# Kernel optimization log

Hardware: AMD Instinct MI355X
Metric: run time of the kernel (lower is better)

The kernel has to match this reference:

```python
import jax, jax.numpy as jnp
import numpy as np

B, S, N = 8, 1024, 1024
IMG_DIM, TXT_DIM = 1024, 768
HEAD_DIM, N_HEADS, N_PROJ = 64, 16, 3
INNER = HEAD_DIM * N_HEADS


def setup_inputs() -> dict:
    key = jax.random.key(0)
    ks = jax.random.split(key, 9)

    def xavier(k, shape):
        fan_out, fan_in = shape[-2], shape[-1]
        limit = float(np.sqrt(6.0 / (fan_in + fan_out)))
        return jax.random.uniform(k, shape, jnp.float32, -limit, limit)

    return {
        "img_tokens": jax.random.normal(ks[0], (B, S, IMG_DIM), jnp.float32),
        "txt_tokens": jax.random.normal(ks[1], (B, N, TXT_DIM), jnp.float32),
        "Wq": xavier(ks[2], (INNER, IMG_DIM)),
        "Wk": xavier(ks[3], (INNER, TXT_DIM)),
        "Wv": xavier(ks[4], (INNER, TXT_DIM)),
        "Wq_banks": xavier(ks[5], (N_PROJ, INNER, IMG_DIM)),
        "Wk_banks": xavier(ks[6], (N_PROJ, INNER, TXT_DIM)),
        "Wrq": xavier(ks[7], (N_PROJ, IMG_DIM)),
        "Wrk": xavier(ks[8], (N_PROJ, TXT_DIM)),
    }


def _ste_argmax_route(scores):
    # forward: hard one-hot; backward: softmax gradient (straight-through)
    soft = jax.nn.softmax(scores, axis=-1)
    one_hot = jax.nn.one_hot(jnp.argmax(scores, axis=-1), scores.shape[-1], dtype=scores.dtype)
    return one_hot + soft - jax.lax.stop_gradient(soft)


def _to_heads(x):
    b, l, _ = x.shape
    return x.reshape(b, l, N_HEADS, HEAD_DIM).transpose(0, 2, 1, 3)  # [B,H,L,d]


def reference(img_tokens, txt_tokens, Wq, Wk, Wv, Wq_banks, Wk_banks, Wrq, Wrk):
    Q = jnp.einsum('bsd,id->bsi', img_tokens, Wq)
    K = jnp.einsum('bnd,id->bni', txt_tokens, Wk)
    V = jnp.einsum('bnd,id->bni', txt_tokens, Wv)

    # Query-side routed redundancy projection
    q_scores = jnp.einsum('bsd,pd->bsp', img_tokens, Wrq)  # [B,S,P]
    q_route = _ste_argmax_route(q_scores)
    q_primes = jnp.einsum('bsd,pid->bsip', img_tokens, Wq_banks)  # [B,S,inner,P]
    Q_prime = jnp.einsum('bsip,bsp->bsi', q_primes, q_route)

    # Key-side routed redundancy projection
    k_scores = jnp.einsum('bnd,pd->bnp', txt_tokens, Wrk)
    k_route = _ste_argmax_route(k_scores)
    k_primes = jnp.einsum('bnd,pid->bnip', txt_tokens, Wk_banks)
    K_prime = jnp.einsum('bnip,bnp->bni', k_primes, k_route)

    return (_to_heads(Q), _to_heads(K), _to_heads(V), _to_heads(Q_prime), _to_heads(K_prime))
```

## Files before the change

### kernel.cpp

```cpp
#include <hip/hip_runtime.h>

typedef unsigned short u16;
typedef unsigned int   u32;
typedef __bf16 bf16x8 __attribute__((ext_vector_type(8)));
typedef float  f32x4  __attribute__((ext_vector_type(4)));

#define DEVI __device__ __forceinline__


DEVI u16 f2bf(float f) {
    u32 u = __float_as_uint(f);
    return (u16)((u + 0x7fffu + ((u >> 16) & 1u)) >> 16);
}
DEVI u32 pk2(float lo, float hi) { return (u32)f2bf(lo) | ((u32)f2bf(hi) << 16); }

DEVI void gload16(const u16* g, u16* s) {
    typedef __attribute__((address_space(1))) const unsigned int GU;
    typedef __attribute__((address_space(3))) unsigned int LU;
    __builtin_amdgcn_global_load_lds((GU*)g, (LU*)s, 16, 0, 0);
}

__global__ __launch_bounds__(512)
void route_fused(const float* __restrict__ img, const float* __restrict__ Wrq,
                 int* __restrict__ cntq, int* __restrict__ qlist, u16* __restrict__ imgB,
                 const float* __restrict__ txt, const float* __restrict__ Wrk,
                 int* __restrict__ cntk, int* __restrict__ klist, u16* __restrict__ txtB)
{
    const float* X; const float* Wr; int D; int* cnt; int* list; u16* Xb; int tokbase;
    if (blockIdx.x < 256) { X = img; Wr = Wrq; D = 1024; cnt = cntq; list = qlist; Xb = imgB; tokbase = blockIdx.x * 32; }
    else                  { X = txt; Wr = Wrk; D = 768;  cnt = cntk; list = klist; Xb = txtB; tokbase = (blockIdx.x - 256) * 32; }

    __shared__ int lcnt[3];
    __shared__ int base[3];
    __shared__ u16 tbank[32];
    __shared__ u16 trank[32];

    const int tid  = threadIdx.x;
    const int lane = tid & 63;
    const int wv   = tid >> 6;
    if (tid < 3) lcnt[tid] = 0;
    __syncthreads();

    const float* w0 = Wr;
    const float* w1 = Wr + D;
    const float* w2 = Wr + 2 * D;

    for (int t = 0; t < 4; ++t) {
        const int ltok = wv * 4 + t;
        const int tok  = tokbase + ltok;
        const float* x = X + (size_t)tok * D;
        u16* xb        = Xb + (size_t)tok * D;
        float a0 = 0.f, a1 = 0.f, a2 = 0.f;
        for (int d = lane * 4; d < D; d += 256) {
            float4 xv = *(const float4*)(x + d);
            uint2 pb = { pk2(xv.x, xv.y), pk2(xv.z, xv.w) };
            *(uint2*)(xb + d) = pb;
            float4 v0 = *(const float4*)(w0 + d);
            float4 v1 = *(const float4*)(w1 + d);
            float4 v2 = *(const float4*)(w2 + d);
            a0 += xv.x * v0.x + xv.y * v0.y + xv.z * v0.z + xv.w * v0.w;
            a1 += xv.x * v1.x + xv.y * v1.y + xv.z * v1.z + xv.w * v1.w;
            a2 += xv.x * v2.x + xv.y * v2.y + xv.z * v2.z + xv.w * v2.w;
        }
#pragma unroll
        for (int m = 32; m; m >>= 1) {
            a0 += __shfl_xor(a0, m);
            a1 += __shfl_xor(a1, m);
            a2 += __shfl_xor(a2, m);
        }
        if (lane == 0) {
            int s = 0; float best = a0;
            if (a1 > best) { best = a1; s = 1; }
            if (a2 > best) { best = a2; s = 2; }
            int r = atomicAdd(&lcnt[s], 1);
            tbank[ltok] = (u16)s;
            trank[ltok] = (u16)r;
        }
    }
    __syncthreads();

    if (tid < 3) base[tid] = atomicAdd(&cnt[tid * 32], lcnt[tid]);
    __syncthreads();

    if (tid < 32) {
        int s = tbank[tid];
        list[s * 8192 + base[s] + trank[tid]] = tokbase + tid;
    }
}

__global__ __launch_bounds__(256)
void cvt_weights(const float* __restrict__ Wq, const float* __restrict__ Wk,
                 const float* __restrict__ Wv, const float* __restrict__ Wqb,
                 const float* __restrict__ Wkb,
                 u16* __restrict__ WqB, u16* __restrict__ WkB, u16* __restrict__ WvB,
                 u16* __restrict__ WqbB, u16* __restrict__ WkbB)
{
    int g = blockIdx.x * 256 + threadIdx.x;
    const float* src; u16* dst; int e;
    if (g < 131072)      { src = Wq;  dst = WqB;  e = g; }
    else if (g < 229376) { src = Wk;  dst = WkB;  e = g - 131072; }
    else if (g < 327680) { src = Wv;  dst = WvB;  e = g - 229376; }
    else if (g < 720896) { src = Wqb; dst = WqbB; e = g - 327680; }
    else                 { src = Wkb; dst = WkbB; e = g - 720896; }
    float4 lo = *(const float4*)(src + (size_t)e * 8);
    float4 hi = *(const float4*)(src + (size_t)e * 8 + 4);
    uint4 p = { pk2(lo.x, lo.y), pk2(lo.z, lo.w), pk2(hi.x, hi.y), pk2(hi.z, hi.w) };
    *(uint4*)(dst + (size_t)e * 8) = p;
}

template <int KD>
DEVI void gemm_core(const u16* gA1, const u16* gA2, const u16* gB1, const u16* gB2,
                    u16* As, u16* Bs, int tid, int wv, int lane, f32x4 (&acc)[4][4])
{
    u16* dA1 = As + 8 * tid;
    u16* dA2 = As + 8 * tid + 2048;
    u16* dB1 = Bs + 8 * tid;
    u16* dB2 = Bs + 8 * tid + 2048;
    const int row15 = lane & 15;
    const int quad  = lane >> 4;
    const int wm = (wv & 1) * 64;
    const int wn = (wv >> 1) * 64;

    for (int k0 = 0; k0 < KD; k0 += 32) {
        gload16(gA1 + k0, dA1);
        gload16(gA2 + k0, dA2);
        gload16(gB1 + k0, dB1);
        gload16(gB2 + k0, dB2);
        __syncthreads();

        bf16x8 a[4], b[4];
#pragma unroll
        for (int i = 0; i < 4; ++i)
            a[i] = *(const bf16x8*)(As + (wm + i * 16 + row15) * 32 + quad * 8);
#pragma unroll
        for (int j = 0; j < 4; ++j)
            b[j] = *(const bf16x8*)(Bs + (wn + j * 16 + row15) * 32 + quad * 8);
#pragma unroll
        for (int i = 0; i < 4; ++i)
#pragma unroll
            for (int j = 0; j < 4; ++j)
                acc[i][j] = __builtin_amdgcn_mfma_f32_16x16x32_bf16(a[i], b[j], acc[i][j], 0, 0, 0);
        __syncthreads();
    }
}

template <int KD>
__global__ __launch_bounds__(256)
void gemm_heads(const u16* __restrict__ A, const u16* __restrict__ W, float* __restrict__ out)
{
    __shared__ __align__(16) u16 As[128 * 32];
    __shared__ __align__(16) u16 Bs[128 * 32];
    const int tid  = threadIdx.x;
    const int lane = tid & 63;
    const int wv   = tid >> 6;
    const int rowbase = blockIdx.x * 128;
    const int nbase   = blockIdx.y * 128;
    const int r1   = tid >> 2;
    const int koff = (tid & 3) * 8;

    const u16* gA1 = A + (size_t)(rowbase + r1) * KD + koff;
    const u16* gA2 = A + (size_t)(rowbase + 64 + r1) * KD + koff;
    const u16* gB1 = W + (size_t)(nbase + r1) * KD + koff;
    const u16* gB2 = W + (size_t)(nbase + 64 + r1) * KD + koff;

    f32x4 acc[4][4];
#pragma unroll
    for (int i = 0; i < 4; ++i)
#pragma unroll
        for (int j = 0; j < 4; ++j)
            acc[i][j] = (f32x4){0.f, 0.f, 0.f, 0.f};

    gemm_core<KD>(gA1, gA2, gB1, gB2, As, Bs, tid, wv, lane, acc);

    const int row15 = lane & 15, quad = lane >> 4;
    const int wm = (wv & 1) * 64, wn = (wv >> 1) * 64;
#pragma unroll
    for (int i = 0; i < 4; ++i) {
#pragma unroll
        for (int r = 0; r < 4; ++r) {
            int m = rowbase + wm + i * 16 + quad * 4 + r;
            int bb = m >> 10, l = m & 1023;
#pragma unroll
            for (int j = 0; j < 4; ++j) {
                int n = nbase + wn + j * 16 + row15;
                size_t off = (((size_t)(bb * 16 + (n >> 6)) * 1024) + l) * 64 + (n & 63);
                out[off] = acc[i][j][r];
            }
        }
    }
}

template <int KD>
__global__ __launch_bounds__(256)
void gemm_prime(const u16* __restrict__ A, const u16* __restrict__ Wb,
                const int* __restrict__ cnt, const int* __restrict__ list,
                float* __restrict__ out)
{
    const int c0 = cnt[0], c1 = cnt[32], c2 = cnt[64];
    const int t0 = (c0 + 127) >> 7, t1 = (c1 + 127) >> 7, t2 = (c2 + 127) >> 7;
    const int rt = blockIdx.x;
    int bank, lt, cb;
    if (rt < t0)                { bank = 0; lt = rt;            cb = c0; }
    else if (rt < t0 + t1)      { bank = 1; lt = rt - t0;       cb = c1; }
    else if (rt < t0 + t1 + t2) { bank = 2; lt = rt - t0 - t1;  cb = c2; }
    else return;

    const int* bl = list + bank * 8192;
    const u16* W = Wb + (size_t)bank * 1024 * KD;

    __shared__ __align__(16) u16 As[128 * 32];
    __shared__ __align__(16) u16 Bs[128 * 32];
    const int tid  = threadIdx.x;
    const int lane = tid & 63;
    const int wv   = tid >> 6;
    const int nbase = blockIdx.y * 128;
    const int r1   = tid >> 2;
    const int koff = (tid & 3) * 8;

    int i1 = lt * 128 + r1;       if (i1 >= cb) i1 = cb - 1;
    int i2 = lt * 128 + 64 + r1;  if (i2 >= cb) i2 = cb - 1;
    const u16* gA1 = A + (size_t)bl[i1] * KD + koff;
    const u16* gA2 = A + (size_t)bl[i2] * KD + koff;
    const u16* gB1 = W + (size_t)(nbase + r1) * KD + koff;
    const u16* gB2 = W + (size_t)(nbase + 64 + r1) * KD + koff;

    f32x4 acc[4][4];
#pragma unroll
    for (int i = 0; i < 4; ++i)
#pragma unroll
        for (int j = 0; j < 4; ++j)
            acc[i][j] = (f32x4){0.f, 0.f, 0.f, 0.f};

    gemm_core<KD>(gA1, gA2, gB1, gB2, As, Bs, tid, wv, lane, acc);

    const int row15 = lane & 15, quad = lane >> 4;
    const int wm = (wv & 1) * 64, wn = (wv >> 1) * 64;
#pragma unroll
    for (int i = 0; i < 4; ++i) {
#pragma unroll
        for (int r = 0; r < 4; ++r) {
            int idx = lt * 128 + wm + i * 16 + quad * 4 + r;
            if (idx < cb) {
                int m = bl[idx];
                int bb = m >> 10, l = m & 1023;
#pragma unroll
                for (int j = 0; j < 4; ++j) {
                    int n = nbase + wn + j * 16 + row15;
                    size_t off = (((size_t)(bb * 16 + (n >> 6)) * 1024) + l) * 64 + (n & 63);
                    out[off] = acc[i][j][r];
                }
            }
        }
    }
}

extern "C" void kernel_launch(void* const* d_in, const int* in_sizes, int n_in,
                              void* d_out, int out_size, void* d_ws, size_t ws_size,
                              hipStream_t stream)
{
    const float* img = (const float*)d_in[0];
    const float* txt = (const float*)d_in[1];
    const float* Wq  = (const float*)d_in[2];
    const float* Wk  = (const float*)d_in[3];
    const float* Wv  = (const float*)d_in[4];
    const float* Wqb = (const float*)d_in[5];
    const float* Wkb = (const float*)d_in[6];
    const float* Wrq = (const float*)d_in[7];
    const float* Wrk = (const float*)d_in[8];
    float* out = (float*)d_out;

    int* cntq  = (int*)d_ws;
    int* cntk  = (int*)d_ws + 128;
    int* qlist = (int*)d_ws + 256;
    int* klist = qlist + 3 * 8192;
    u16* imgB  = (u16*)((char*)d_ws + (1 << 18));
    u16* txtB  = imgB + (size_t)8192 * 1024;
    u16* WqB   = txtB + (size_t)8192 * 768;
    u16* WkB   = WqB  + (size_t)1024 * 1024;
    u16* WvB   = WkB  + (size_t)1024 * 768;
    u16* WqbB  = WvB  + (size_t)1024 * 768;
    u16* WkbB  = WqbB + (size_t)3 * 1024 * 1024;

    const size_t OSZ = (size_t)8 * 16 * 1024 * 64;

    hipMemsetAsync(d_ws, 0, 1024, stream);

    route_fused<<<512, 512, 0, stream>>>(img, Wrq, cntq, qlist, imgB,
                                         txt, Wrk, cntk, klist, txtB);
    cvt_weights<<<3968, 256, 0, stream>>>(Wq, Wk, Wv, Wqb, Wkb,
                                          WqB, WkB, WvB, WqbB, WkbB);

    gemm_heads<1024><<<dim3(64, 8), 256, 0, stream>>>(imgB, WqB, out);
    gemm_heads<768> <<<dim3(64, 8), 256, 0, stream>>>(txtB, WkB, out + OSZ);
    gemm_heads<768> <<<dim3(64, 8), 256, 0, stream>>>(txtB, WvB, out + 2 * OSZ);

    gemm_prime<1024><<<dim3(66, 8), 256, 0, stream>>>(imgB, WqbB, cntq, qlist, out + 3 * OSZ);
    gemm_prime<768> <<<dim3(66, 8), 256, 0, stream>>>(txtB, WkbB, cntk, klist, out + 4 * OSZ);
}
```

Before: 414.0 us.

## Merge GEMMs into one launch, deepen K tile to 64 with swizzled LDS

Weight conversion now runs inside the routing kernel as extra blocks, and the five GEMMs (three dense head projections, two routed bank projections) run as a single persistent-grid launch that dispatches on block index. The GEMM core now loads 64-wide K slices, halving barrier count per tile, and XOR-swizzles the LDS layout to avoid bank conflicts on fragment reads. This cuts launch overhead and tail gaps between kernels at the cost of doubled shared memory per block, which may lower occupancy.

```diff
diff --git a/kernel.cpp b/kernel.cpp
--- a/kernel.cpp
+++ b/kernel.cpp
@@ -21,11 +21,33 @@
 }
 
 __global__ __launch_bounds__(512)
-void route_fused(const float* __restrict__ img, const float* __restrict__ Wrq,
-                 int* __restrict__ cntq, int* __restrict__ qlist, u16* __restrict__ imgB,
-                 const float* __restrict__ txt, const float* __restrict__ Wrk,
-                 int* __restrict__ cntk, int* __restrict__ klist, u16* __restrict__ txtB)
-{
+void route_cvt(const float* __restrict__ img, const float* __restrict__ Wrq,
+               int* __restrict__ cntq, int* __restrict__ qlist, u16* __restrict__ imgB,
+               const float* __restrict__ txt, const float* __restrict__ Wrk,
+               int* __restrict__ cntk, int* __restrict__ klist, u16* __restrict__ txtB,
+               const float* __restrict__ Wq, const float* __restrict__ Wk,
+               const float* __restrict__ Wv, const float* __restrict__ Wqb,
+               const float* __restrict__ Wkb,
+               u16* __restrict__ WqB, u16* __restrict__ WkB, u16* __restrict__ WvB,
+               u16* __restrict__ WqbB, u16* __restrict__ WkbB)
+{
+    const int tid = threadIdx.x;
+
+    if (blockIdx.x >= 512) {
+        int g = (blockIdx.x - 512) * 512 + tid;
+        const float* src; u16* dst; int e;
+        if (g < 131072)      { src = Wq;  dst = WqB;  e = g; }
+        else if (g < 229376) { src = Wk;  dst = WkB;  e = g - 131072; }
+        else if (g < 327680) { src = Wv;  dst = WvB;  e = g - 229376; }
+        else if (g < 720896) { src = Wqb; dst = WqbB; e = g - 327680; }
+        else                 { src = Wkb; dst = WkbB; e = g - 720896; }
+        float4 lo = *(const float4*)(src + (size_t)e * 8);
+        float4 hi = *(const float4*)(src + (size_t)e * 8 + 4);
+        uint4 p = { pk2(lo.x, lo.y), pk2(lo.z, lo.w), pk2(hi.x, hi.y), pk2(hi.z, hi.w) };
+        *(uint4*)(dst + (size_t)e * 8) = p;
+        return;
+    }
+
     const float* X; const float* Wr; int D; int* cnt; int* list; u16* Xb; int tokbase;
     if (blockIdx.x < 256) { X = img; Wr = Wrq; D = 1024; cnt = cntq; list = qlist; Xb = imgB; tokbase = blockIdx.x * 32; }
     else                  { X = txt; Wr = Wrk; D = 768;  cnt = cntk; list = klist; Xb = txtB; tokbase = (blockIdx.x - 256) * 32; }
@@ -35,7 +57,6 @@
     __shared__ u16 tbank[32];
     __shared__ u16 trank[32];
 
-    const int tid  = threadIdx.x;
     const int lane = tid & 63;
     const int wv   = tid >> 6;
     if (tid < 3) lcnt[tid] = 0;
@@ -88,89 +109,85 @@
     }
 }
 
-__global__ __launch_bounds__(256)
-void cvt_weights(const float* __restrict__ Wq, const float* __restrict__ Wk,
-                 const float* __restrict__ Wv, const float* __restrict__ Wqb,
-                 const float* __restrict__ Wkb,
-                 u16* __restrict__ WqB, u16* __restrict__ WkB, u16* __restrict__ WvB,
-                 u16* __restrict__ WqbB, u16* __restrict__ WkbB)
-{
-    int g = blockIdx.x * 256 + threadIdx.x;
-    const float* src; u16* dst; int e;
-    if (g < 131072)      { src = Wq;  dst = WqB;  e = g; }
-    else if (g < 229376) { src = Wk;  dst = WkB;  e = g - 131072; }
-    else if (g < 327680) { src = Wv;  dst = WvB;  e = g - 229376; }
-    else if (g < 720896) { src = Wqb; dst = WqbB; e = g - 327680; }
-    else                 { src = Wkb; dst = WkbB; e = g - 720896; }
-    float4 lo = *(const float4*)(src + (size_t)e * 8);
-    float4 hi = *(const float4*)(src + (size_t)e * 8 + 4);
-    uint4 p = { pk2(lo.x, lo.y), pk2(lo.z, lo.w), pk2(hi.x, hi.y), pk2(hi.z, hi.w) };
-    *(uint4*)(dst + (size_t)e * 8) = p;
-}
-
 template <int KD>
-DEVI void gemm_core(const u16* gA1, const u16* gA2, const u16* gB1, const u16* gB2,
-                    u16* As, u16* Bs, int tid, int wv, int lane, f32x4 (&acc)[4][4])
-{
-    u16* dA1 = As + 8 * tid;
-    u16* dA2 = As + 8 * tid + 2048;
-    u16* dB1 = Bs + 8 * tid;
-    u16* dB2 = Bs + 8 * tid + 2048;
+DEVI void gemm_core64(const u16* a0, const u16* a1, const u16* a2, const u16* a3,
+                      const u16* b0, const u16* b1, const u16* b2, const u16* b3,
+                      u16* As, u16* Bs, int tid, int wv, int lane, f32x4 (&acc)[4][4])
+{
+    u16* dA = As + 8 * tid;
+    u16* dB = Bs + 8 * tid;
     const int row15 = lane & 15;
     const int quad  = lane >> 4;
     const int wm = (wv & 1) * 64;
     const int wn = (wv >> 1) * 64;
 
-    for (int k0 = 0; k0 < KD; k0 += 32) {
-        gload16(gA1 + k0, dA1);
-        gload16(gA2 + k0, dA2);
-        gload16(gB1 + k0, dB1);
-        gload16(gB2 + k0, dB2);
+    for (int k0 = 0; k0 < KD; k0 += 64) {
+        gload16(a0 + k0, dA);
+        gload16(a1 + k0, dA + 2048);
+        gload16(a2 + k0, dA + 4096);
+        gload16(a3 + k0, dA + 6144);
+        gload16(b0 + k0, dB);
+        gload16(b1 + k0, dB + 2048);
+        gload16(b2 + k0, dB + 4096);
+        gload16(b3 + k0, dB + 6144);
         __syncthreads();
 
-        bf16x8 a[4], b[4];
-#pragma unroll
-        for (int i = 0; i < 4; ++i)
-            a[i] = *(const bf16x8*)(As + (wm + i * 16 + row15) * 32 + quad * 8);
+#pragma unroll
+        for (int kk = 0; kk < 64; kk += 32) {
+            bf16x8 a[4], b[4];
+            const int sw = (kk >> 3) + quad;
+#pragma unroll
+            for (int i = 0; i < 4; ++i) {
+                const int row = wm + i * 16 + row15;
+                a[i] = *(const bf16x8*)(As + row * 64 + ((sw ^ (row & 7)) << 3));
+            }
+#pragma unroll
+            for (int j = 0; j < 4; ++j) {
+                const int row = wn + j * 16 + row15;
+                b[j] = *(const bf16x8*)(Bs + row * 64 + ((sw ^ (row & 7)) << 3));
+            }
+#pragma unroll
+            for (int i = 0; i < 4; ++i)
+#pragma unroll
+                for (int j = 0; j < 4; ++j)
+                    acc[i][j] = __builtin_amdgcn_mfma_f32_16x16x32_bf16(a[i], b[j], acc[i][j], 0, 0, 0);
+        }
+        __syncthreads();
+    }
+}
+
+DEVI void acc_init(f32x4 (&acc)[4][4]) {
+#pragma unroll
+    for (int i = 0; i < 4; ++i)
 #pragma unroll
         for (int j = 0; j < 4; ++j)
-            b[j] = *(const bf16x8*)(Bs + (wn + j * 16 + row15) * 32 + quad * 8);
-#pragma unroll
-        for (int i = 0; i < 4; ++i)
-#pragma unroll
-            for (int j = 0; j < 4; ++j)
-                acc[i][j] = __builtin_amdgcn_mfma_f32_16x16x32_bf16(a[i], b[j], acc[i][j], 0, 0, 0);
-        __syncthreads();
-    }
+            acc[i][j] = (f32x4){0.f, 0.f, 0.f, 0.f};
 }
 
 template <int KD>
-__global__ __launch_bounds__(256)
-void gemm_heads(const u16* __restrict__ A, const u16* __restrict__ W, float* __restrict__ out)
-{
-    __shared__ __align__(16) u16 As[128 * 32];
-    __shared__ __align__(16) u16 Bs[128 * 32];
+DEVI void gemm_heads_body(const u16* __restrict__ A, const u16* __restrict__ W,
+                          float* __restrict__ out, int lbid, u16* As, u16* Bs)
+{
     const int tid  = threadIdx.x;
     const int lane = tid & 63;
     const int wv   = tid >> 6;
-    const int rowbase = blockIdx.x * 128;
-    const int nbase   = blockIdx.y * 128;
-    const int r1   = tid >> 2;
-    const int koff = (tid & 3) * 8;
-
-    const u16* gA1 = A + (size_t)(rowbase + r1) * KD + koff;
-    const u16* gA2 = A + (size_t)(rowbase + 64 + r1) * KD + koff;
-    const u16* gB1 = W + (size_t)(nbase + r1) * KD + koff;
-    const u16* gB2 = W + (size_t)(nbase + 64 + r1) * KD + koff;
+    const int rowbase = (lbid >> 3) * 128;
+    const int nbase   = (lbid & 7) * 128;
+    const int r0 = tid >> 3;
+    const int sg = ((tid & 7) ^ (r0 & 7)) * 8;
+
+    const u16* gA0 = A + (size_t)(rowbase + r0)      * KD + sg;
+    const u16* gA1 = A + (size_t)(rowbase + r0 + 32) * KD + sg;
+    const u16* gA2 = A + (size_t)(rowbase + r0 + 64) * KD + sg;
+    const u16* gA3 = A + (size_t)(rowbase + r0 + 96) * KD + sg;
+    const u16* gB0 = W + (size_t)(nbase + r0)        * KD + sg;
+    const u16* gB1 = W + (size_t)(nbase + r0 + 32)   * KD + sg;
+    const u16* gB2 = W + (size_t)(nbase + r0 + 64)   * KD + sg;
+    const u16* gB3 = W + (size_t)(nbase + r0 + 96)   * KD + sg;
 
     f32x4 acc[4][4];
-#pragma unroll
-    for (int i = 0; i < 4; ++i)
-#pragma unroll
-        for (int j = 0; j < 4; ++j)
-            acc[i][j] = (f32x4){0.f, 0.f, 0.f, 0.f};
-
-    gemm_core<KD>(gA1, gA2, gB1, gB2, As, Bs, tid, wv, lane, acc);
+    acc_init(acc);
+    gemm_core64<KD>(gA0, gA1, gA2, gA3, gB0, gB1, gB2, gB3, As, Bs, tid, wv, lane, acc);
 
     const int row15 = lane & 15, quad = lane >> 4;
     const int wm = (wv & 1) * 64, wn = (wv >> 1) * 64;
@@ -191,14 +208,13 @@
 }
 
 template <int KD>
-__global__ __launch_bounds__(256)
-void gemm_prime(const u16* __restrict__ A, const u16* __restrict__ Wb,
-                const int* __restrict__ cnt, const int* __restrict__ list,
-                float* __restrict__ out)
+DEVI void gemm_prime_body(const u16* __restrict__ A, const u16* __restrict__ Wb,
+                          const int* __restrict__ cnt, const int* __restrict__ list,
+                          float* __restrict__ out, int lbid, u16* As, u16* Bs)
 {
     const int c0 = cnt[0], c1 = cnt[32], c2 = cnt[64];
     const int t0 = (c0 + 127) >> 7, t1 = (c1 + 127) >> 7, t2 = (c2 + 127) >> 7;
-    const int rt = blockIdx.x;
+    const int rt = lbid >> 3;
     int bank, lt, cb;
     if (rt < t0)                { bank = 0; lt = rt;            cb = c0; }
     else if (rt < t0 + t1)      { bank = 1; lt = rt - t0;       cb = c1; }
@@ -208,30 +224,29 @@
     const int* bl = list + bank * 8192;
     const u16* W = Wb + (size_t)bank * 1024 * KD;
 
-    __shared__ __align__(16) u16 As[128 * 32];
-    __shared__ __align__(16) u16 Bs[128 * 32];
     const int tid  = threadIdx.x;
     const int lane = tid & 63;
     const int wv   = tid >> 6;
-    const int nbase = blockIdx.y * 128;
-    const int r1   = tid >> 2;
-    const int koff = (tid & 3) * 8;
-
-    int i1 = lt * 128 + r1;       if (i1 >= cb) i1 = cb - 1;
-    int i2 = lt * 128 + 64 + r1;  if (i2 >= cb) i2 = cb - 1;
-    const u16* gA1 = A + (size_t)bl[i1] * KD + koff;
-    const u16* gA2 = A + (size_t)bl[i2] * KD + koff;
-    const u16* gB1 = W + (size_t)(nbase + r1) * KD + koff;
-    const u16* gB2 = W + (size_t)(nbase + 64 + r1) * KD + koff;
+    const int nbase = (lbid & 7) * 128;
+    const int r0 = tid >> 3;
+    const int sg = ((tid & 7) ^ (r0 & 7)) * 8;
+
+    int i0 = lt * 128 + r0;       if (i0 >= cb) i0 = cb - 1;
+    int i1 = lt * 128 + r0 + 32;  if (i1 >= cb) i1 = cb - 1;
+    int i2 = lt * 128 + r0 + 64;  if (i2 >= cb) i2 = cb - 1;
+    int i3 = lt * 128 + r0 + 96;  if (i3 >= cb) i3 = cb - 1;
+    const u16* gA0 = A + (size_t)bl[i0] * KD + sg;
+    const u16* gA1 = A + (size_t)bl[i1] * KD + sg;
+    const u16* gA2 = A + (size_t)bl[i2] * KD + sg;
+    const u16* gA3 = A + (size_t)bl[i3] * KD + sg;
+    const u16* gB0 = W + (size_t)(nbase + r0)      * KD + sg;
+    const u16* gB1 = W + (size_t)(nbase + r0 + 32) * KD + sg;
+    const u16* gB2 = W + (size_t)(nbase + r0 + 64) * KD + sg;
+    const u16* gB3 = W + (size_t)(nbase + r0 + 96) * KD + sg;
 
     f32x4 acc[4][4];
-#pragma unroll
-    for (int i = 0; i < 4; ++i)
-#pragma unroll
-        for (int j = 0; j < 4; ++j)
-            acc[i][j] = (f32x4){0.f, 0.f, 0.f, 0.f};
-
-    gemm_core<KD>(gA1, gA2, gB1, gB2, As, Bs, tid, wv, lane, acc);
+    acc_init(acc);
+    gemm_core64<KD>(gA0, gA1, gA2, gA3, gB0, gB1, gB2, gB3, As, Bs, tid, wv, lane, acc);
 
     const int row15 = lane & 15, quad = lane >> 4;
     const int wm = (wv & 1) * 64, wn = (wv >> 1) * 64;
@@ -252,6 +267,32 @@
             }
         }
     }
+}
+
+__global__ __launch_bounds__(256)
+void gemm_all(const u16* __restrict__ imgB, const u16* __restrict__ txtB,
+              const u16* __restrict__ WqB, const u16* __restrict__ WkB,
+              const u16* __restrict__ WvB, const u16* __restrict__ WqbB,
+              const u16* __restrict__ WkbB,
+              const int* __restrict__ cntq, const int* __restrict__ qlist,
+              const int* __restrict__ cntk, const int* __restrict__ klist,
+              float* __restrict__ out)
+{
+    __shared__ __align__(16) u16 As[128 * 64];
+    __shared__ __align__(16) u16 Bs[128 * 64];
+    const size_t OSZ = (size_t)8 * 16 * 1024 * 64;
+    const int bid = blockIdx.x;
+
+    if (bid < 528)
+        gemm_prime_body<1024>(imgB, WqbB, cntq, qlist, out + 3 * OSZ, bid, As, Bs);
+    else if (bid < 1040)
+        gemm_heads_body<1024>(imgB, WqB, out, bid - 528, As, Bs);
+    else if (bid < 1568)
+        gemm_prime_body<768>(txtB, WkbB, cntk, klist, out + 4 * OSZ, bid - 1040, As, Bs);
+    else if (bid < 2080)
+        gemm_heads_body<768>(txtB, WkB, out + OSZ, bid - 1568, As, Bs);
+    else
+        gemm_heads_body<768>(txtB, WvB, out + 2 * OSZ, bid - 2080, As, Bs);
 }
 
 extern "C" void kernel_launch(void* const* d_in, const int* in_sizes, int n_in,
@@ -281,19 +322,13 @@
     u16* WqbB  = WvB  + (size_t)1024 * 768;
     u16* WkbB  = WqbB + (size_t)3 * 1024 * 1024;
 
-    const size_t OSZ = (size_t)8 * 16 * 1024 * 64;
-
     hipMemsetAsync(d_ws, 0, 1024, stream);
 
-    route_fused<<<512, 512, 0, stream>>>(img, Wrq, cntq, qlist, imgB,
-                                         txt, Wrk, cntk, klist, txtB);
-    cvt_weights<<<3968, 256, 0, stream>>>(Wq, Wk, Wv, Wqb, Wkb,
-                                          WqB, WkB, WvB, WqbB, WkbB);
-
-    gemm_heads<1024><<<dim3(64, 8), 256, 0, stream>>>(imgB, WqB, out);
-    gemm_heads<768> <<<dim3(64, 8), 256, 0, stream>>>(txtB, WkB, out + OSZ);
-    gemm_heads<768> <<<dim3(64, 8), 256, 0, stream>>>(txtB, WvB, out + 2 * OSZ);
-
-    gemm_prime<1024><<<dim3(66, 8), 256, 0, stream>>>(imgB, WqbB, cntq, qlist, out + 3 * OSZ);
-    gemm_prime<768> <<<dim3(66, 8), 256, 0, stream>>>(txtB, WkbB, cntk, klist, out + 4 * OSZ);
-}
+    route_cvt<<<2496, 512, 0, stream>>>(img, Wrq, cntq, qlist, imgB,
+                                        txt, Wrk, cntk, klist, txtB,
+                                        Wq, Wk, Wv, Wqb, Wkb,
+                                        WqB, WkB, WvB, WqbB, WkbB);
+
+    gemm_all<<<2592, 256, 0, stream>>>(imgB, txtB, WqB, WkB, WvB, WqbB, WkbB,
+                                       cntq, qlist, cntk, klist, out);
+}
```

Result: faster. 353.8 us (-14.5%).
